# Performance work log

Measured on AMD Instinct MI355X. Metric: run time of the kernel, lower is better.

The kernel has to match this reference:

```python
import jax, jax.numpy as jnp
import numpy as np

N = 100_000      # nodes
E = 1_600_000    # edges (avg degree 16)
D_IN, D_HID, D_OUT = 128, 64, 64
NEG_SLOPE = 0.2  # PyG GATConv default


def setup_inputs() -> dict:
    key = jax.random.key(0)
    ks = jax.random.split(key, 10)
    s = lambda k, shape: jax.random.normal(k, shape, jnp.float32) * 0.1
    return {
        "x": jax.random.normal(ks[0], (N, D_IN), jnp.float32),
        "edge_index": jax.random.randint(ks[1], (2, E), 0, N, dtype=jnp.int32),
        "W1": s(ks[2], (D_IN, D_HID)),
        "a_src1": s(ks[3], (D_HID,)),
        "a_dst1": s(ks[4], (D_HID,)),
        "b1": jnp.zeros((D_HID,), jnp.float32),
        "W2": s(ks[5], (D_HID, D_OUT)),
        "a_src2": s(ks[6], (D_OUT,)),
        "a_dst2": s(ks[7], (D_OUT,)),
        "b2": jnp.zeros((D_OUT,), jnp.float32),
    }


def gat_conv(x, src, dst, W, a_src, a_dst, b):
    """Single-head PyG-style GATConv (self-loops already appended to src/dst)."""
    n = x.shape[0]
    h = x @ W                                   # [N, D]
    # per-edge attention logits: leaky_relu(a_src . h_j + a_dst . h_i)
    logit = jax.nn.leaky_relu((h @ a_src)[src] + (h @ a_dst)[dst], NEG_SLOPE)
    # segment softmax over incoming edges of each dst node
    m = jax.ops.segment_max(logit, dst, num_segments=n)
    e = jnp.exp(logit - m[dst])
    denom = jax.ops.segment_sum(e, dst, num_segments=n)
    alpha = e / (denom[dst] + 1e-16)            # [E]
    out = jax.ops.segment_sum(alpha[:, None] * h[src], dst, num_segments=n)
    return out + b


def reference(x, edge_index, W1, a_src1, a_dst1, b1, W2, a_src2, a_dst2, b2):
    n = x.shape[0]
    loops = jnp.arange(n, dtype=edge_index.dtype)  # add_self_loops=True default
    src = jnp.concatenate([edge_index[0], loops])
    dst = jnp.concatenate([edge_index[1], loops])
    h = gat_conv(x, src, dst, W1, a_src1, a_dst1, b1)
    embedding = jax.nn.relu(h)   # dropout = identity (inference semantics)
    out = gat_conv(embedding, src, dst, W2, a_src2, a_dst2, b2)
    return (embedding, out)
```

## Files before the change

kernel.cpp:

```cpp
#include <hip/hip_runtime.h>
#include <hip/hip_bf16.h>

#define DHID 64
#define SUBSH 9
#define SUBSZ (1 << SUBSH)
#define PCAP 16384
#define EB 2048
typedef __attribute__((ext_vector_type(8))) short short8;
typedef __attribute__((ext_vector_type(4))) float f32x4;

static __device__ __forceinline__ short tobf(float f) {
  __hip_bfloat16 h = __float2bfloat16(f);
  return *reinterpret_cast<short*>(&h);
}

__global__ __launch_bounds__(256)
void k_fusedA(const int* __restrict__ src, const int* __restrict__ dst,
              int* __restrict__ bkt, int* __restrict__ bcnt,
              int E, int nsb, int cap, int nbkt,
              const float* __restrict__ xf, const float* __restrict__ W1,
              const float* __restrict__ a_s, const float* __restrict__ a_d,
              short* __restrict__ hb, float* __restrict__ asb,
              float* __restrict__ adb, int N) {
  __shared__ int lcnt[256];
  __shared__ int lbase[256];
  __shared__ __align__(16) short ldsB[64 * 128];
  int tid = threadIdx.x;
  if (blockIdx.x < nbkt) {
    int c0 = blockIdx.x * EB;
    for (int i = tid; i < nsb; i += 256) lcnt[i] = 0;
    __syncthreads();
    int wloc[8], uloc[8], rloc[8];
    #pragma unroll
    for (int k = 0; k < 8; k++) {
      int i = c0 + tid + k * 256;
      if (i < E) {
        int d = dst[i];
        int w = d >> SUBSH;
        wloc[k] = w;
        uloc[k] = (src[i] << SUBSH) | (d & (SUBSZ - 1));
        rloc[k] = atomicAdd(&lcnt[w], 1);
      } else wloc[k] = -1;
    }
    __syncthreads();
    for (int i = tid; i < nsb; i += 256) lbase[i] = atomicAdd(&bcnt[i], lcnt[i]);
    __syncthreads();
    #pragma unroll
    for (int k = 0; k < 8; k++) {
      int w = wloc[k];
      if (w >= 0) bkt[(size_t)w * cap + lbase[w] + rloc[k]] = uloc[k];
    }
    return;
  }
  int n0 = (blockIdx.x - nbkt) * 64;
  for (int e = tid; e < 128 * 64; e += 256) {
    int k = e >> 6, c = e & 63;
    ldsB[c * 128 + (k ^ ((c & 7) << 3))] = tobf(W1[e]);
  }
  __syncthreads();

  int l = tid & 63, w = tid >> 6;
  int c = l & 15, g = l >> 4;
  f32x4 acc[4];
  #pragma unroll
  for (int t = 0; t < 4; t++) acc[t] = (f32x4){0.f, 0.f, 0.f, 0.f};

  int arow = 16 * w + c;
  int row0 = n0 + arow;
  const float* xr = xf + (size_t)row0 * 128;
  bool okr = row0 < N;
  short8 afr[4];
  #pragma unroll
  for (int s = 0; s < 4; s++) {
    int ke = s * 32 + g * 8;
    float4 u0 = make_float4(0.f, 0.f, 0.f, 0.f), u1 = u0;
    if (okr) { u0 = *(const float4*)(xr + ke); u1 = *(const float4*)(xr + ke + 4); }
    short8 af;
    af[0] = tobf(u0.x); af[1] = tobf(u0.y); af[2] = tobf(u0.z); af[3] = tobf(u0.w);
    af[4] = tobf(u1.x); af[5] = tobf(u1.y); af[6] = tobf(u1.z); af[7] = tobf(u1.w);
    afr[s] = af;
  }
  #pragma unroll
  for (int s = 0; s < 4; s++) {
    int ke = s * 32 + g * 8;
    #pragma unroll
    for (int t = 0; t < 4; t++) {
      int bcol = 16 * t + c;
      short8 bf = *(const short8*)(ldsB + bcol * 128 + (ke ^ ((bcol & 7) << 3)));
      acc[t] = __builtin_amdgcn_mfma_f32_16x16x32_bf16(afr[s], bf, acc[t], 0, 0, 0);
    }
  }
  float av_s[4], av_d[4];
  #pragma unroll
  for (int t = 0; t < 4; t++) { av_s[t] = a_s[16 * t + c]; av_d[t] = a_d[16 * t + c]; }
  #pragma unroll
  for (int q = 0; q < 4; q++) {
    int row = n0 + 16 * w + g * 4 + q;
    bool ok = row < N;
    float rs = 0.f, rd = 0.f;
    #pragma unroll
    for (int t = 0; t < 4; t++) {
      float v = acc[t][q];
      if (ok) hb[(size_t)row * 64 + 16 * t + c] = tobf(v);
      rs += v * av_s[t]; rd += v * av_d[t];
    }
    #pragma unroll
    for (int off = 1; off < 16; off <<= 1) {
      rs += __shfl_xor(rs, off, 64);
      rd += __shfl_xor(rd, off, 64);
    }
    if (ok && c == 0) { asb[row] = rs; adb[row] = rd; }
  }
}

__global__ __launch_bounds__(256)
void k_place2(const int* __restrict__ bkt, const int* __restrict__ bcnt,
              int* __restrict__ roff, int* __restrict__ csr,
              int N, int nsb, int cap) {
  __shared__ int scanbuf[256];
  __shared__ int h[SUBSZ];
  __shared__ int roff_l[SUBSZ + 1];
  __shared__ int lcnt[SUBSZ];
  __shared__ int stage[PCAP];
  __shared__ int sbase;
  int sb = blockIdx.x, tid = threadIdx.x;
  int d0 = sb << SUBSH;
  int nn = min(N - d0, SUBSZ);

  int tot = 0;
  if (tid < nsb) tot = bcnt[tid] + min(N - (tid << SUBSH), SUBSZ);
  scanbuf[tid] = tot; __syncthreads();
  for (int off = 1; off < 256; off <<= 1) {
    int t = (tid >= off) ? scanbuf[tid - off] : 0;
    __syncthreads(); scanbuf[tid] += t; __syncthreads();
  }
  if (tid == sb) sbase = scanbuf[tid] - tot;
  __syncthreads();

  for (int j = tid; j < SUBSZ; j += 256) { h[j] = 1; lcnt[j] = 0; }
  __syncthreads();
  int nE = bcnt[sb];
  const int* b = bkt + (size_t)sb * cap;
  for (int i = tid; i < nE; i += 256) atomicAdd(&h[b[i] & (SUBSZ - 1)], 1);
  __syncthreads();

  int a0 = h[2 * tid], a1 = h[2 * tid + 1];
  int s = a0 + a1;
  scanbuf[tid] = s; __syncthreads();
  for (int off = 1; off < 256; off <<= 1) {
    int t = (tid >= off) ? scanbuf[tid - off] : 0;
    __syncthreads(); scanbuf[tid] += t; __syncthreads();
  }
  int excl = sbase + scanbuf[tid] - s;
  roff_l[2 * tid] = excl;
  roff_l[2 * tid + 1] = excl + a0;
  if (tid == 255) roff_l[SUBSZ] = sbase + scanbuf[255];
  __syncthreads();

  for (int j = tid; j < nn; j += 256) roff[d0 + j] = roff_l[j];
  if (d0 + nn == N && tid == 0) roff[N] = roff_l[nn];

  int base0 = roff_l[0];
  int span = roff_l[nn] - base0;
  if (span <= PCAP) {
    for (int d = tid; d < nn; d += 256) stage[roff_l[d] - base0] = (d0 + d) << 7;
    for (int i = tid; i < nE; i += 256) {
      int u = b[i];
      int dl = u & (SUBSZ - 1);
      int rk = 1 + atomicAdd(&lcnt[dl], 1);
      stage[roff_l[dl] - base0 + rk] = (u >> SUBSH) << 7;
    }
    __syncthreads();
    for (int j = tid; j < span; j += 256) csr[base0 + j] = stage[j];
  } else {
    for (int d = tid; d < nn; d += 256) csr[roff_l[d]] = (d0 + d) << 7;
    for (int i = tid; i < nE; i += 256) {
      int u = b[i];
      int dl = u & (SUBSZ - 1);
      int rk = 1 + atomicAdd(&lcnt[dl], 1);
      csr[roff_l[dl] + rk] = (u >> SUBSH) << 7;
    }
  }
}

__global__ __launch_bounds__(256)
void k_mgemm2(const short* __restrict__ eb, const float* __restrict__ W2,
              const float* __restrict__ a_s, const float* __restrict__ a_d,
              short* __restrict__ hb, float* __restrict__ asb,
              float* __restrict__ adb, int N) {
  __shared__ __align__(16) short lds[64 * 64 * 2];
  int tid = threadIdx.x;
  int n0 = blockIdx.x * 64;
  const char* ga = (const char*)eb + (size_t)n0 * 128;
  #pragma unroll
  for (int j = 0; j < 2; j++) {
    int d = j * 4096 + tid * 16;
    __builtin_amdgcn_global_load_lds(
        (__attribute__((address_space(1))) const void*)(ga + d),
        (__attribute__((address_space(3))) void*)((char*)lds + d), 16, 0, 0);
  }
  short* B = lds + 64 * 64;
  for (int e = tid; e < 64 * 64; e += 256) {
    int k = e >> 6, c = e & 63;
    B[c * 64 + (k ^ ((c & 7) << 3))] = tobf(W2[e]);
  }
  __syncthreads();

  int l = tid & 63, w = tid >> 6;
  int c = l & 15, g = l >> 4;
  const short* A = lds;
  f32x4 acc[4];
  #pragma unroll
  for (int t = 0; t < 4; t++) acc[t] = (f32x4){0.f, 0.f, 0.f, 0.f};
  int arow = 16 * w + c;
  #pragma unroll
  for (int s = 0; s < 2; s++) {
    int ke = s * 32 + g * 8;
    short8 af = *(const short8*)(A + arow * 64 + (ke ^ ((arow & 7) << 3)));
    #pragma unroll
    for (int t = 0; t < 4; t++) {
      int bcol = 16 * t + c;
      short8 bf = *(const short8*)(B + bcol * 64 + (ke ^ ((bcol & 7) << 3)));
      acc[t] = __builtin_amdgcn_mfma_f32_16x16x32_bf16(af, bf, acc[t], 0, 0, 0);
    }
  }
  float av_s[4], av_d[4];
  #pragma unroll
  for (int t = 0; t < 4; t++) { av_s[t] = a_s[16 * t + c]; av_d[t] = a_d[16 * t + c]; }
  #pragma unroll
  for (int q = 0; q < 4; q++) {
    int row = n0 + 16 * w + g * 4 + q;
    bool ok = row < N;
    float rs = 0.f, rd = 0.f;
    #pragma unroll
    for (int t = 0; t < 4; t++) {
      float v = acc[t][q];
      if (ok) hb[(size_t)row * 64 + 16 * t + c] = tobf(v);
      rs += v * av_s[t]; rd += v * av_d[t];
    }
    #pragma unroll
    for (int off = 1; off < 16; off <<= 1) {
      rs += __shfl_xor(rs, off, 64);
      rd += __shfl_xor(rd, off, 64);
    }
    if (ok && c == 0) { asb[row] = rs; adb[row] = rd; }
  }
}

__global__ void k_agg(const int* __restrict__ roff, const int* __restrict__ csr,
                      const float* __restrict__ asb, const float* __restrict__ adb,
                      const short* __restrict__ hb, const float* __restrict__ b,
                      float* __restrict__ out, short* __restrict__ outb,
                      int N, int relu) {
  const char* hbase = (const char*)hb;
  int lane = threadIdx.x & 63;
  int colb = (lane & 15) * 8;
  int L = lane & 15;
  int wid = blockIdx.x * (blockDim.x >> 6) + (threadIdx.x >> 6);
  int nw = gridDim.x * (blockDim.x >> 6);
  float4 bv4 = ((const float4*)b)[L];
  for (int n = wid; n < N; n += nw) {
    int r0 = roff[n], r1 = roff[n + 1];
    float adn = adb[n];
    float a0 = 0.f, a1 = 0.f, a2 = 0.f, a3 = 0.f, denl = 0.f;
    for (int base = r0; base < r1; base += 64) {
      int cnt = min(64, r1 - base);
      int s128 = 0; float e = 0.f;
      if (lane < cnt) {
        s128 = csr[base + lane];
        float l = asb[s128 >> 7] + adn;
        l = fmaxf(l, 0.2f * l);
        e = __expf(l);
      }
      denl += e;
      int cntUp = (cnt + 3) & ~3;
      int addrv = (lane >> 4) << 2;
      #pragma unroll 8
      for (int j = 0; j < cntUp; j += 4) {
        int sofs = __builtin_amdgcn_ds_bpermute(addrv, s128);
        int ewi  = __builtin_amdgcn_ds_bpermute(addrv, (int)__float_as_uint(e));
        addrv += 16;
        float ew = __uint_as_float((unsigned)ewi);
        uint2 u = *(const uint2*)(hbase + (unsigned)(sofs + colb));
        a0 = fmaf(__uint_as_float(u.x << 16), ew, a0);
        a1 = fmaf(__uint_as_float(u.x & 0xFFFF0000u), ew, a1);
        a2 = fmaf(__uint_as_float(u.y << 16), ew, a2);
        a3 = fmaf(__uint_as_float(u.y & 0xFFFF0000u), ew, a3);
      }
    }
    #pragma unroll
    for (int off = 16; off <= 32; off <<= 1) {
      a0 += __shfl_xor(a0, off, 64); a1 += __shfl_xor(a1, off, 64);
      a2 += __shfl_xor(a2, off, 64); a3 += __shfl_xor(a3, off, 64);
    }
    float den = denl;
    #pragma unroll
    for (int off = 32; off; off >>= 1) den += __shfl_xor(den, off, 64);
    float inv = 1.f / (den + 1e-16f);
    if (lane < 16) {
      float4 o;
      o.x = fmaf(a0, inv, bv4.x); o.y = fmaf(a1, inv, bv4.y);
      o.z = fmaf(a2, inv, bv4.z); o.w = fmaf(a3, inv, bv4.w);
      if (relu) {
        o.x = fmaxf(o.x, 0.f); o.y = fmaxf(o.y, 0.f);
        o.z = fmaxf(o.z, 0.f); o.w = fmaxf(o.w, 0.f);
      }
      ((float4*)(out + (size_t)n * DHID))[L] = o;
      if (outb) {
        short4 ob = make_short4(tobf(o.x), tobf(o.y), tobf(o.z), tobf(o.w));
        ((short4*)(outb + (size_t)n * DHID))[L ^ ((n & 7) << 1)] = ob;
      }
    }
  }
}

extern "C" void kernel_launch(void* const* d_in, const int* in_sizes, int n_in,
                              void* d_out, int out_size, void* d_ws, size_t ws_size,
                              hipStream_t stream) {
  const float* x   = (const float*)d_in[0];
  const int*   ei  = (const int*)d_in[1];
  const float* W1  = (const float*)d_in[2];
  const float* as1 = (const float*)d_in[3];
  const float* ad1 = (const float*)d_in[4];
  const float* b1  = (const float*)d_in[5];
  const float* W2  = (const float*)d_in[6];
  const float* as2 = (const float*)d_in[7];
  const float* ad2 = (const float*)d_in[8];
  const float* b2  = (const float*)d_in[9];

  int N = in_sizes[0] / 128;
  int E = in_sizes[1] / 2;
  const int* srcp = ei;
  const int* dstp = ei + E;

  float* emb  = (float*)d_out;
  float* out2 = emb + (size_t)N * DHID;

  char* w = (char*)d_ws;
  auto alloc = [&](size_t bytes) { char* p = w; w += (bytes + 255) & ~(size_t)255; return p; };
  int NR = ((N + 63) / 64) * 64;
  int* roff = (int*)alloc((size_t)(N + 1) * 4);
  int* csr  = (int*)alloc((size_t)(E + N) * 4);
  int* bcnt = (int*)alloc(1024);
  char* scr0 = alloc((size_t)NR * 128 * 2);
  short* hb = (short*)alloc((size_t)NR * 64 * 2);
  float* asb = (float*)alloc((size_t)N * 4);
  float* adb = (float*)alloc((size_t)N * 4);
  short* eb = (short*)scr0;
  int* bkt  = (int*)scr0;

  int nsb = (N + SUBSZ - 1) >> SUBSH;
  int cap = E / nsb + 4096;

  int NBLK = (N + 63) / 64;
  int nbkt = (E + EB - 1) / EB;

  hipMemsetAsync(bcnt, 0, (size_t)nsb * 4, stream);
  k_fusedA<<<nbkt + NBLK, 256, 0, stream>>>(srcp, dstp, bkt, bcnt, E, nsb, cap, nbkt,
                                            x, W1, as1, ad1, hb, asb, adb, N);
  k_place2<<<nsb, 256, 0, stream>>>(bkt, bcnt, roff, csr, N, nsb, cap);

  k_agg<<<2048, 256, 0, stream>>>(roff, csr, asb, adb, hb, b1, emb, eb, N, 1);
  k_mgemm2<<<NBLK, 256, 0, stream>>>(eb, W2, as2, ad2, hb, asb, adb, N);
  k_agg<<<2048, 256, 0, stream>>>(roff, csr, asb, adb, hb, b2, out2, (short*)nullptr, N, 0);
}
```

Before: 173.8 us.

## Software-pipeline node metadata and neighbor loads across iterations in aggregation kernel

The aggregation kernel now prefetches row offsets, dst attention scalars, CSR neighbor indices and source attention values for the next one to two nodes the wave will process. This overlaps the dependent chain roff→csr→asb with the current node's gather, hiding latency of the serial loads. It costs extra registers, which may reduce occupancy, and special-cases the first 64-edge chunk separately from the rest.

```diff
diff --git a/kernel.cpp b/kernel.cpp
--- a/kernel.cpp
+++ b/kernel.cpp
@@ -259,26 +259,64 @@
   int wid = blockIdx.x * (blockDim.x >> 6) + (threadIdx.x >> 6);
   int nw = gridDim.x * (blockDim.x >> 6);
   float4 bv4 = ((const float4*)b)[L];
+
+  int r0c = 0, r1c = 0, sc = 0, r0n = 0, r1n = 0, sn = 0;
+  float adc = 0.f, avc = 0.f, adn = 0.f;
+  if (wid < N) {
+    r0c = roff[wid]; r1c = roff[wid + 1]; adc = adb[wid];
+    if (lane < min(64, r1c - r0c)) sc = csr[r0c + lane];
+    avc = asb[sc >> 7];
+  }
+  if (wid + nw < N) {
+    r0n = roff[wid + nw]; r1n = roff[wid + nw + 1]; adn = adb[wid + nw];
+    if (lane < min(64, r1n - r0n)) sn = csr[r0n + lane];
+  }
+
   for (int n = wid; n < N; n += nw) {
-    int r0 = roff[n], r1 = roff[n + 1];
-    float adn = adb[n];
-    float a0 = 0.f, a1 = 0.f, a2 = 0.f, a3 = 0.f, denl = 0.f;
-    for (int base = r0; base < r1; base += 64) {
-      int cnt = min(64, r1 - base);
-      int s128 = 0; float e = 0.f;
+    int cnt0 = min(64, r1c - r0c);
+    float e = 0.f;
+    if (lane < cnt0) {
+      float l = avc + adc;
+      l = fmaxf(l, 0.2f * l);
+      e = __expf(l);
+    }
+    int n2 = n + 2 * nw;
+    int r02 = 0, r12 = 0; float ad2 = 0.f;
+    if (n2 < N) { r02 = roff[n2]; r12 = roff[n2 + 1]; ad2 = adb[n2]; }
+    float avn = asb[sn >> 7];
+
+    float a0 = 0.f, a1 = 0.f, a2 = 0.f, a3 = 0.f, denl = e;
+    {
+      int cntUp = (cnt0 + 3) & ~3;
+      int addrv = (lane >> 4) << 2;
+      #pragma unroll 4
+      for (int j = 0; j < cntUp; j += 4) {
+        int sofs = __builtin_amdgcn_ds_bpermute(addrv, sc);
+        int ewi  = __builtin_amdgcn_ds_bpermute(addrv, (int)__float_as_uint(e));
+        addrv += 16;
+        float ew = __uint_as_float((unsigned)ewi);
+        uint2 u = *(const uint2*)(hbase + (unsigned)(sofs + colb));
+        a0 = fmaf(__uint_as_float(u.x << 16), ew, a0);
+        a1 = fmaf(__uint_as_float(u.x & 0xFFFF0000u), ew, a1);
+        a2 = fmaf(__uint_as_float(u.y << 16), ew, a2);
+        a3 = fmaf(__uint_as_float(u.y & 0xFFFF0000u), ew, a3);
+      }
+    }
+    for (int base = r0c + 64; base < r1c; base += 64) {
+      int cnt = min(64, r1c - base);
+      int s128 = 0; float e2 = 0.f;
       if (lane < cnt) {
         s128 = csr[base + lane];
-        float l = asb[s128 >> 7] + adn;
+        float l = asb[s128 >> 7] + adc;
         l = fmaxf(l, 0.2f * l);
-        e = __expf(l);
+        e2 = __expf(l);
       }
-      denl += e;
+      denl += e2;
       int cntUp = (cnt + 3) & ~3;
       int addrv = (lane >> 4) << 2;
-      #pragma unroll 8
       for (int j = 0; j < cntUp; j += 4) {
         int sofs = __builtin_amdgcn_ds_bpermute(addrv, s128);
-        int ewi  = __builtin_amdgcn_ds_bpermute(addrv, (int)__float_as_uint(e));
+        int ewi  = __builtin_amdgcn_ds_bpermute(addrv, (int)__float_as_uint(e2));
         addrv += 16;
         float ew = __uint_as_float((unsigned)ewi);
         uint2 u = *(const uint2*)(hbase + (unsigned)(sofs + colb));
@@ -311,6 +349,10 @@
         ((short4*)(outb + (size_t)n * DHID))[L ^ ((n & 7) << 1)] = ob;
       }
     }
+    r0c = r0n; r1c = r1n; adc = adn; sc = sn; avc = avn;
+    r0n = r02; r1n = r12; adn = ad2;
+    sn = 0;
+    if (n2 < N && lane < min(64, r1n - r0n)) sn = csr[r0n + lane];
   }
 }
 
```

Result: faster. 164.0 us (-5.6%).
